# Kernel tuning notes

Measured on AMD Instinct MI355X. Metric: run time of the kernel, lower is better.

## Reference

```python
import jax, jax.numpy as jnp
import numpy as np

N_NODES = 20000
N_EDGES = 160000
F_IN = 512
HIDDEN = 512
N_CLASSES = 40


def setup_inputs() -> dict:
    key = jax.random.key(0)
    k1, k2, k3, k4 = jax.random.split(key, 4)
    x = jax.random.normal(k1, (N_NODES, F_IN), dtype=jnp.float32)
    edge_index = jax.random.randint(k2, (2, N_EDGES), 0, N_NODES, dtype=jnp.int64)
    # Glorot-ish init scale for the linear weights
    W1 = jax.random.normal(k3, (F_IN, HIDDEN), dtype=jnp.float32) / np.sqrt(F_IN)
    b1 = jnp.zeros((HIDDEN,), dtype=jnp.float32)
    W2 = jax.random.normal(k4, (HIDDEN, N_CLASSES), dtype=jnp.float32) / np.sqrt(HIDDEN)
    b2 = jnp.zeros((N_CLASSES,), dtype=jnp.float32)
    return {"x": x, "edge_index": edge_index, "W1": W1, "b1": b1, "W2": W2, "b2": b2}


def _gcn_conv(x, W, b, src, dst, n_nodes):
    """PyG GCNConv: h = D^-1/2 (A+I) D^-1/2 (x W) + b, self-loops already in src/dst."""
    h = x @ W  # [N, out]
    deg = jax.ops.segment_sum(jnp.ones_like(dst, dtype=h.dtype), dst, num_segments=n_nodes)
    deg_inv_sqrt = jnp.where(deg > 0, jax.lax.rsqrt(jnp.maximum(deg, 1.0)), 0.0)
    norm = deg_inv_sqrt[src] * deg_inv_sqrt[dst]  # [E]
    msg = h[src] * norm[:, None]  # [E, out]
    return jax.ops.segment_sum(msg, dst, num_segments=n_nodes) + b


def reference(x, edge_index, W1, b1, W2, b2):
    n = x.shape[0]
    loop = jnp.arange(n, dtype=edge_index.dtype)
    src = jnp.concatenate([edge_index[0], loop])  # add self-loops
    dst = jnp.concatenate([edge_index[1], loop])
    h = _gcn_conv(x, W1, b1, src, dst, n)
    h = jax.nn.relu(h)
    # dropout(p=0.5) is identity in eval mode
    out = _gcn_conv(h, W2, b2, src, dst, n)
    return out
```

## Files before the change

kernel.cpp:

```cpp
#include <hip/hip_runtime.h>
#include <hip/hip_bf16.h>
#include <stdint.h>

#define N_NODES  20000
#define N_EDGES  160000
#define N_CLS    40
#define M_PAD    20096
#define CNT_PAD  20480
#define CAP      64

typedef __bf16 bf16;
typedef __attribute__((ext_vector_type(8))) __bf16 bf16x8;
typedef __attribute__((ext_vector_type(4))) float floatx4;

__device__ inline floatx4 zero4() { floatx4 z = {0.f, 0.f, 0.f, 0.f}; return z; }

typedef __attribute__((address_space(3))) uint32_t lds_u32;
typedef __attribute__((address_space(1))) const uint32_t glb_u32;
__device__ inline void ldst16(const bf16* g, bf16* l) {
    __builtin_amdgcn_global_load_lds((glb_u32*)g, (lds_u32*)l, 16, 0, 0);
}

struct Params {
    const float* x; const int* ei; const float* W1; const float* b1;
    const float* W2; const float* b2; float* out;
    bf16 *xb, *w1t, *w2p, *h1; float* h2;
    int *cnt, *colb;
};

#define S0_ZERO 20
#define S0_CONV 5024
#define S0_W1T  128
#define S0_W2P  96
#define S0_TOT  (S0_ZERO + S0_CONV + S0_W1T + S0_W2P)
#define NB_G1   640
#define NB_FILL 625

__global__ __launch_bounds__(256) void k_s0(Params p) {
    const int vb = blockIdx.x, tid = threadIdx.x;
    if (vb < S0_ZERO) {
        int4* dz = (int4*)(p.cnt) + vb * 256 + tid;
        *dz = make_int4(0, 0, 0, 0);
    } else if (vb < S0_ZERO + S0_CONV) {
        long e0 = ((long)(vb - S0_ZERO) * 256 + tid) * 8;
        int row = (int)(e0 >> 9);
        bf16x8 v;
        if (row < N_NODES) {
            const float4* ptr = (const float4*)(p.x + e0);
            float4 f0 = ptr[0], f1 = ptr[1];
            v[0] = (bf16)f0.x; v[1] = (bf16)f0.y; v[2] = (bf16)f0.z; v[3] = (bf16)f0.w;
            v[4] = (bf16)f1.x; v[5] = (bf16)f1.y; v[6] = (bf16)f1.z; v[7] = (bf16)f1.w;
        } else {
            for (int j = 0; j < 8; ++j) v[j] = (bf16)0.f;
        }
        *(bf16x8*)(p.xb + e0) = v;
    } else if (vb < S0_ZERO + S0_CONV + S0_W1T) {
        int t  = (vb - S0_ZERO - S0_CONV) * 256 + tid;
        int n  = t & 511;
        int k0 = (t >> 9) * 8;
        bf16x8 v;
        for (int j = 0; j < 8; ++j) v[j] = (bf16)p.W1[((k0 + j) << 9) + n];
        *(bf16x8*)(p.w1t + n * 512 + k0) = v;
    } else {
        int t = (vb - S0_ZERO - S0_CONV - S0_W1T) * 256 + tid;
        int j = t & 7; int e = t >> 3;
        int lane = e & 63; e >>= 6;
        int nb = e % 3; int kt = e / 3;
        int k = kt * 32 + (lane >> 4) * 8 + j;
        int n = nb * 16 + (lane & 15);
        float v = (n < N_CLS) ? p.W2[k * N_CLS + n] : 0.f;
        p.w2p[t] = (bf16)v;
    }
}

__global__ __launch_bounds__(256) void k_g1f(Params p) {
    if (blockIdx.x >= NB_G1) {
        int e = (blockIdx.x - NB_G1) * 256 + threadIdx.x;
        if (e < N_EDGES) {
            int d = p.ei[N_EDGES + e];
            int j = atomicAdd(&p.cnt[d], 1);
            if (j < CAP) p.colb[d * CAP + j] = p.ei[e];
        }
        return;
    }
    const int g  = blockIdx.x;
    const int mi = (g >> 5) * 8 + (g & 7);
    const int ni = (g >> 3) & 3;
    if (mi >= 157) return;
    __shared__ bf16 As[2][128 * 32];
    __shared__ bf16 Bs[2][128 * 32];
    const int tid  = threadIdx.x;
    const int lane = tid & 63;
    const int w    = tid >> 6;
    const int wm   = w >> 1, wn = w & 1;
    const int m0   = mi * 128;
    const int n0   = ni * 128;
    const int fr   = lane & 15, fq = lane >> 4;

    floatx4 acc[4][4];
    for (int mb = 0; mb < 4; ++mb)
        for (int nb = 0; nb < 4; ++nb) acc[mb][nb] = zero4();

    const int sr = lane >> 2;
    const int sk = (((lane & 3) ^ ((lane >> 3) & 3))) * 8;
    const bf16* Ag = p.xb  + (long)(m0 + w * 32 + sr) * 512 + sk;
    const bf16* Bg = p.w1t + (long)(n0 + w * 32 + sr) * 512 + sk;
    const int wof = w * 1024;

    ldst16(Ag,            As[0] + wof);
    ldst16(Ag + 16 * 512, As[0] + wof + 512);
    ldst16(Bg,            Bs[0] + wof);
    ldst16(Bg + 16 * 512, Bs[0] + wof + 512);

    const int fqs = (fq ^ ((fr >> 1) & 3)) * 8;

    for (int kt = 0; kt < 16; ++kt) {
        const int cur = kt & 1, nxt = cur ^ 1;
        __syncthreads();
        if (kt < 15) {
            const int k1 = (kt + 1) * 32;
            ldst16(Ag + k1,            As[nxt] + wof);
            ldst16(Ag + k1 + 16 * 512, As[nxt] + wof + 512);
            ldst16(Bg + k1,            Bs[nxt] + wof);
            ldst16(Bg + k1 + 16 * 512, Bs[nxt] + wof + 512);
        }
        bf16x8 af[4], bfv[4];
        for (int mb = 0; mb < 4; ++mb)
            af[mb]  = *(const bf16x8*)(As[cur] + (wm * 64 + mb * 16 + fr) * 32 + fqs);
        for (int nb = 0; nb < 4; ++nb)
            bfv[nb] = *(const bf16x8*)(Bs[cur] + (wn * 64 + nb * 16 + fr) * 32 + fqs);
        for (int mb = 0; mb < 4; ++mb)
            for (int nb = 0; nb < 4; ++nb)
                acc[mb][nb] = __builtin_amdgcn_mfma_f32_16x16x32_bf16(af[mb], bfv[nb], acc[mb][nb], 0, 0, 0);
    }
    for (int mb = 0; mb < 4; ++mb)
        for (int nb = 0; nb < 4; ++nb) {
            int row0 = m0 + wm * 64 + mb * 16 + fq * 4;
            int c    = n0 + wn * 64 + nb * 16 + fr;
            for (int r = 0; r < 4; ++r)
                p.h1[(long)(row0 + r) * 512 + c] = (bf16)acc[mb][nb][r];
        }
}

__global__ __launch_bounds__(256) void k_agg1g2(Params p) {
    __shared__ bf16 t[16 * 512];
    const int tid = threadIdx.x, l = tid & 63, w = tid >> 6;
    const int ib = blockIdx.x * 16;

    const float4* bp = (const float4*)(p.b1 + l * 8);
    float4 c0 = bp[0], c1 = bp[1];
    float bb[8] = {c0.x, c0.y, c0.z, c0.w, c1.x, c1.y, c1.z, c1.w};

    for (int q4 = 0; q4 < 4; ++q4) {
        const int r = w * 4 + q4;
        const int i = ib + r;
        bf16x8 o;
        if (i >= N_NODES) {
            for (int j = 0; j < 8; ++j) o[j] = (bf16)0.f;
        } else {
            const int ci = p.cnt[i];
            const float di = rsqrtf((float)(ci + 1));
            float acc[8];
            {
                bf16x8 v = *(const bf16x8*)(p.h1 + (long)i * 512 + l * 8);
                const float wi = di * di;
                for (int j = 0; j < 8; ++j) acc[j] = (float)v[j] * wi;
            }
            const int e1 = ci < CAP ? ci : CAP;
            const int* rowcol = p.colb + (long)i * CAP;
            int e = 0;
            for (; e + 8 <= e1; e += 8) {
                int4 sa = *(const int4*)(rowcol + e);
                int4 sb = *(const int4*)(rowcol + e + 4);
                float wgt[8];
                wgt[0] = rsqrtf((float)(p.cnt[sa.x] + 1)) * di;
                wgt[1] = rsqrtf((float)(p.cnt[sa.y] + 1)) * di;
                wgt[2] = rsqrtf((float)(p.cnt[sa.z] + 1)) * di;
                wgt[3] = rsqrtf((float)(p.cnt[sa.w] + 1)) * di;
                wgt[4] = rsqrtf((float)(p.cnt[sb.x] + 1)) * di;
                wgt[5] = rsqrtf((float)(p.cnt[sb.y] + 1)) * di;
                wgt[6] = rsqrtf((float)(p.cnt[sb.z] + 1)) * di;
                wgt[7] = rsqrtf((float)(p.cnt[sb.w] + 1)) * di;
                bf16x8 u[8];
                u[0] = *(const bf16x8*)(p.h1 + (long)sa.x * 512 + l * 8);
                u[1] = *(const bf16x8*)(p.h1 + (long)sa.y * 512 + l * 8);
                u[2] = *(const bf16x8*)(p.h1 + (long)sa.z * 512 + l * 8);
                u[3] = *(const bf16x8*)(p.h1 + (long)sa.w * 512 + l * 8);
                u[4] = *(const bf16x8*)(p.h1 + (long)sb.x * 512 + l * 8);
                u[5] = *(const bf16x8*)(p.h1 + (long)sb.y * 512 + l * 8);
                u[6] = *(const bf16x8*)(p.h1 + (long)sb.z * 512 + l * 8);
                u[7] = *(const bf16x8*)(p.h1 + (long)sb.w * 512 + l * 8);
                for (int q = 0; q < 8; ++q)
                    for (int j = 0; j < 8; ++j) acc[j] += (float)u[q][j] * wgt[q];
            }
            for (; e + 4 <= e1; e += 4) {
                int4 ss = *(const int4*)(rowcol + e);
                float w0 = rsqrtf((float)(p.cnt[ss.x] + 1)) * di;
                float w1 = rsqrtf((float)(p.cnt[ss.y] + 1)) * di;
                float w2 = rsqrtf((float)(p.cnt[ss.z] + 1)) * di;
                float w3 = rsqrtf((float)(p.cnt[ss.w] + 1)) * di;
                bf16x8 u0 = *(const bf16x8*)(p.h1 + (long)ss.x * 512 + l * 8);
                bf16x8 u1 = *(const bf16x8*)(p.h1 + (long)ss.y * 512 + l * 8);
                bf16x8 u2 = *(const bf16x8*)(p.h1 + (long)ss.z * 512 + l * 8);
                bf16x8 u3 = *(const bf16x8*)(p.h1 + (long)ss.w * 512 + l * 8);
                for (int j = 0; j < 8; ++j)
                    acc[j] += (float)u0[j] * w0 + (float)u1[j] * w1 + (float)u2[j] * w2 + (float)u3[j] * w3;
            }
            for (; e < e1; ++e) {
                int s = rowcol[e];
                float wt = rsqrtf((float)(p.cnt[s] + 1)) * di;
                bf16x8 u = *(const bf16x8*)(p.h1 + (long)s * 512 + l * 8);
                for (int j = 0; j < 8; ++j) acc[j] += (float)u[j] * wt;
            }
            for (int j = 0; j < 8; ++j) {
                float f = acc[j] + bb[j];
                f = f > 0.f ? f : 0.f;
                o[j] = (bf16)f;
            }
        }
        *(bf16x8*)((char*)t + r * 1024 + ((l * 16) ^ ((r & 7) << 4))) = o;
    }
    __syncthreads();
    if (w < 3) {
        const int fr = l & 15, fq = l >> 4;
        const int nb = w;
        floatx4 acc2 = zero4();
        for (int kt = 0; kt < 16; ++kt) {
            bf16x8 af = *(const bf16x8*)((const char*)t + fr * 1024 +
                                         ((kt * 64 + fq * 16) ^ ((fr & 7) << 4)));
            bf16x8 bfr = *(const bf16x8*)(p.w2p + ((kt * 3 + nb) * 64 + l) * 8);
            acc2 = __builtin_amdgcn_mfma_f32_16x16x32_bf16(af, bfr, acc2, 0, 0, 0);
        }
        for (int r2 = 0; r2 < 4; ++r2)
            p.h2[(long)(ib + fq * 4 + r2) * 48 + nb * 16 + fr] = acc2[r2];
    }
}

__global__ __launch_bounds__(256) void k_agg2(Params p) {
    const int i = blockIdx.x * 4 + (threadIdx.x >> 6);
    const int l = threadIdx.x & 63;
    if (i >= N_NODES || l >= N_CLS) return;
    const int ci = p.cnt[i];
    const float di = rsqrtf((float)(ci + 1));
    float acc = p.h2[(long)i * 48 + l] * di * di;
    const int e1 = ci < CAP ? ci : CAP;
    const int* rowcol = p.colb + (long)i * CAP;
    int e = 0;
    for (; e + 4 <= e1; e += 4) {
        int4 ss = *(const int4*)(rowcol + e);
        acc += p.h2[(long)ss.x * 48 + l] * (rsqrtf((float)(p.cnt[ss.x] + 1)) * di)
             + p.h2[(long)ss.y * 48 + l] * (rsqrtf((float)(p.cnt[ss.y] + 1)) * di)
             + p.h2[(long)ss.z * 48 + l] * (rsqrtf((float)(p.cnt[ss.z] + 1)) * di)
             + p.h2[(long)ss.w * 48 + l] * (rsqrtf((float)(p.cnt[ss.w] + 1)) * di);
    }
    for (; e < e1; ++e) {
        int s = rowcol[e];
        acc += p.h2[(long)s * 48 + l] * (rsqrtf((float)(p.cnt[s] + 1)) * di);
    }
    p.out[(long)i * N_CLS + l] = acc + p.b2[l];
}


extern "C" void kernel_launch(void* const* d_in, const int* in_sizes, int n_in,
                              void* d_out, int out_size, void* d_ws, size_t ws_size,
                              hipStream_t stream) {
    Params p;
    p.x  = (const float*)d_in[0];
    p.ei = (const int*)d_in[1];
    p.W1 = (const float*)d_in[2];
    p.b1 = (const float*)d_in[3];
    p.W2 = (const float*)d_in[4];
    p.b2 = (const float*)d_in[5];
    p.out = (float*)d_out;

    char* base = (char*)d_ws;
    size_t o = 0;
    auto alloc = [&](size_t bytes) { size_t r = o; o = (o + bytes + 255) & ~(size_t)255; return r; };
    p.xb   = (bf16*)(base + alloc((size_t)M_PAD * 512 * 2));
    p.w1t  = (bf16*)(base + alloc((size_t)512 * 512 * 2));
    p.w2p  = (bf16*)(base + alloc((size_t)24576 * 2));
    p.h1   = (bf16*)(base + alloc((size_t)M_PAD * 512 * 2));
    p.h2   = (float*)(base + alloc((size_t)M_PAD * 48 * 4));
    p.cnt  = (int*)(base + alloc((size_t)CNT_PAD * 4));
    p.colb = (int*)(base + alloc((size_t)N_NODES * CAP * 4));

    k_s0    <<<S0_TOT,           256, 0, stream>>>(p);
    k_g1f   <<<NB_G1 + NB_FILL,  256, 0, stream>>>(p);
    k_agg1g2<<<M_PAD / 16,       256, 0, stream>>>(p);
    k_agg2  <<<N_NODES / 4,      256, 0, stream>>>(p);
}
```

Baseline: 151.9 us.

## Triple-buffer GEMM1 LDS tiles with explicit vmcnt waits and barriers

Replaces the double-buffered LDS pipeline in the first GEMM with a three-stage ring buffer that prefetches two k-tiles ahead. It uses explicit s_waitcnt vmcnt and raw s_barrier in place of __syncthreads, so loads stay in flight across iterations. It also adds unroll pragmas. The aim is to hide global-to-LDS latency better, at the cost of 50% more LDS per block, which may lower occupancy.

```diff
diff --git a/kernel.cpp b/kernel.cpp
--- a/kernel.cpp
+++ b/kernel.cpp
@@ -17,7 +17,7 @@
 
 typedef __attribute__((address_space(3))) uint32_t lds_u32;
 typedef __attribute__((address_space(1))) const uint32_t glb_u32;
-__device__ inline void ldst16(const bf16* g, bf16* l) {
+__device__ inline void ldst16(const void* g, void* l) {
     __builtin_amdgcn_global_load_lds((glb_u32*)g, (lds_u32*)l, 16, 0, 0);
 }
 
@@ -87,8 +87,8 @@
     const int mi = (g >> 5) * 8 + (g & 7);
     const int ni = (g >> 3) & 3;
     if (mi >= 157) return;
-    __shared__ bf16 As[2][128 * 32];
-    __shared__ bf16 Bs[2][128 * 32];
+    __shared__ bf16 As[3 * 4096];
+    __shared__ bf16 Bs[3 * 4096];
     const int tid  = threadIdx.x;
     const int lane = tid & 63;
     const int w    = tid >> 6;
@@ -98,7 +98,9 @@
     const int fr   = lane & 15, fq = lane >> 4;
 
     floatx4 acc[4][4];
+#pragma unroll
     for (int mb = 0; mb < 4; ++mb)
+#pragma unroll
         for (int nb = 0; nb < 4; ++nb) acc[mb][nb] = zero4();
 
     const int sr = lane >> 2;
@@ -107,36 +109,55 @@
     const bf16* Bg = p.w1t + (long)(n0 + w * 32 + sr) * 512 + sk;
     const int wof = w * 1024;
 
-    ldst16(Ag,            As[0] + wof);
-    ldst16(Ag + 16 * 512, As[0] + wof + 512);
-    ldst16(Bg,            Bs[0] + wof);
-    ldst16(Bg + 16 * 512, Bs[0] + wof + 512);
+    ldst16(Ag,                 As + wof);
+    ldst16(Ag + 16 * 512,      As + wof + 512);
+    ldst16(Bg,                 Bs + wof);
+    ldst16(Bg + 16 * 512,      Bs + wof + 512);
+    ldst16(Ag + 32,            As + 4096 + wof);
+    ldst16(Ag + 32 + 16 * 512, As + 4096 + wof + 512);
+    ldst16(Bg + 32,            Bs + 4096 + wof);
+    ldst16(Bg + 32 + 16 * 512, Bs + 4096 + wof + 512);
 
     const int fqs = (fq ^ ((fr >> 1) & 3)) * 8;
 
     for (int kt = 0; kt < 16; ++kt) {
-        const int cur = kt & 1, nxt = cur ^ 1;
-        __syncthreads();
         if (kt < 15) {
-            const int k1 = (kt + 1) * 32;
-            ldst16(Ag + k1,            As[nxt] + wof);
-            ldst16(Ag + k1 + 16 * 512, As[nxt] + wof + 512);
-            ldst16(Bg + k1,            Bs[nxt] + wof);
-            ldst16(Bg + k1 + 16 * 512, Bs[nxt] + wof + 512);
-        }
+            asm volatile("s_waitcnt vmcnt(4)" ::: "memory");
+        } else {
+            asm volatile("s_waitcnt vmcnt(0)" ::: "memory");
+        }
+        __builtin_amdgcn_sched_barrier(0);
+        __builtin_amdgcn_s_barrier();
+        __builtin_amdgcn_sched_barrier(0);
+        if (kt < 14) {
+            const int bo = ((kt + 2) % 3) * 4096;
+            const int k2 = (kt + 2) * 32;
+            ldst16(Ag + k2,            As + bo + wof);
+            ldst16(Ag + k2 + 16 * 512, As + bo + wof + 512);
+            ldst16(Bg + k2,            Bs + bo + wof);
+            ldst16(Bg + k2 + 16 * 512, Bs + bo + wof + 512);
+        }
+        const int co = (kt % 3) * 4096;
         bf16x8 af[4], bfv[4];
+#pragma unroll
         for (int mb = 0; mb < 4; ++mb)
-            af[mb]  = *(const bf16x8*)(As[cur] + (wm * 64 + mb * 16 + fr) * 32 + fqs);
+            af[mb]  = *(const bf16x8*)(As + co + (wm * 64 + mb * 16 + fr) * 32 + fqs);
+#pragma unroll
         for (int nb = 0; nb < 4; ++nb)
-            bfv[nb] = *(const bf16x8*)(Bs[cur] + (wn * 64 + nb * 16 + fr) * 32 + fqs);
+            bfv[nb] = *(const bf16x8*)(Bs + co + (wn * 64 + nb * 16 + fr) * 32 + fqs);
+#pragma unroll
         for (int mb = 0; mb < 4; ++mb)
+#pragma unroll
             for (int nb = 0; nb < 4; ++nb)
                 acc[mb][nb] = __builtin_amdgcn_mfma_f32_16x16x32_bf16(af[mb], bfv[nb], acc[mb][nb], 0, 0, 0);
     }
+#pragma unroll
     for (int mb = 0; mb < 4; ++mb)
+#pragma unroll
         for (int nb = 0; nb < 4; ++nb) {
             int row0 = m0 + wm * 64 + mb * 16 + fq * 4;
             int c    = n0 + wn * 64 + nb * 16 + fr;
+#pragma unroll
             for (int r = 0; r < 4; ++r)
                 p.h1[(long)(row0 + r) * 512 + c] = (bf16)acc[mb][nb][r];
         }
```

After: 154.6 us. No clear change (+1.8%).
